# Kernel tuning notes

Measured on AMD Instinct MI355X. Metric: run time of the kernel, lower is better.

The kernel has to match this reference:

```python
import jax, jax.numpy as jnp
import numpy as np

N = 50000      # nodes
E = 800000     # edges
F_IN = 128     # n_features
H = 4          # n_heads
C1 = 64        # n_hidden (per-head out of layer 1)
C2 = 32        # n_classes (per-head out of layer 2)
NEG_SLOPE = 0.2
EPS = 1e-16


def setup_inputs() -> dict:
    key = jax.random.key(0)
    ks = jax.random.split(key, 12)
    x = jax.random.normal(ks[0], (N, F_IN), dtype=jnp.float32)
    edge_index = jax.random.randint(ks[1], (2, E), 0, N, dtype=jnp.int64)
    # layer 1 params (GATConv: shared lin for src/dst, att_src/att_dst vectors, bias)
    W1 = jax.random.normal(ks[2], (F_IN, H * C1), dtype=jnp.float32) * (1.0 / np.sqrt(F_IN))
    att_src1 = jax.random.normal(ks[3], (H, C1), dtype=jnp.float32) * 0.1
    att_dst1 = jax.random.normal(ks[4], (H, C1), dtype=jnp.float32) * 0.1
    b1 = jnp.zeros((C1,), dtype=jnp.float32)
    # layer 2 params
    W2 = jax.random.normal(ks[5], (C1, H * C2), dtype=jnp.float32) * (1.0 / np.sqrt(C1))
    att_src2 = jax.random.normal(ks[6], (H, C2), dtype=jnp.float32) * 0.1
    att_dst2 = jax.random.normal(ks[7], (H, C2), dtype=jnp.float32) * 0.1
    b2 = jnp.zeros((C2,), dtype=jnp.float32)
    return {"x": x, "edge_index": edge_index,
            "W1": W1, "att_src1": att_src1, "att_dst1": att_dst1, "b1": b1,
            "W2": W2, "att_src2": att_src2, "att_dst2": att_dst2, "b2": b2}


def gat_conv(x, src, dst, W, att_src, att_dst, b, heads, out_ch):
    """PyG GATConv with concat=False (head-averaged output)."""
    n = x.shape[0]
    h = (x @ W).reshape(n, heads, out_ch)                 # [N, H, C]
    a_s = jnp.einsum('nhc,hc->nh', h, att_src)            # [N, H]
    a_d = jnp.einsum('nhc,hc->nh', h, att_dst)            # [N, H]
    e = jax.nn.leaky_relu(a_s[src] + a_d[dst], NEG_SLOPE)  # [E, H]
    # segment softmax over edges grouped by destination node
    m = jax.ops.segment_max(e, dst, num_segments=n)        # [N, H]
    m = jnp.where(jnp.isfinite(m), m, 0.0)
    ex = jnp.exp(e - m[dst])                               # [E, H]
    denom = jax.ops.segment_sum(ex, dst, num_segments=n)   # [N, H]
    alpha = ex / (denom[dst] + EPS)                        # [E, H]
    # scatter-add aggregation of attended source features
    msg = alpha[:, :, None] * h[src]                       # [E, H, C]
    out = jax.ops.segment_sum(msg, dst, num_segments=n)    # [N, H, C]
    return out.mean(axis=1) + b                            # [N, C]


def reference(x, edge_index, W1, att_src1, att_dst1, b1, W2, att_src2, att_dst2, b2):
    src, dst = edge_index[0], edge_index[1]
    h = jax.nn.relu(gat_conv(x, src, dst, W1, att_src1, att_dst1, b1, H, C1))
    # dropout is identity in eval mode
    out = gat_conv(h, src, dst, W2, att_src2, att_dst2, b2, H, C2)
    return out
```

## Files before the change

kernel.cpp:

```cpp
#include <hip/hip_runtime.h>
#include <hip/hip_fp16.h>
#include <cstdint>
#include <cstddef>

#define N_NODES 50000
#define N_EDGES 800000
#define F_IN 128
#define H_HEADS 4
#define C1 64
#define C2 32
#define NEG_SLOPE 0.2f
#define EPS_GAT 1e-16f
#define SLOT_CAP 96
#define FILL_BPG 256
#define NODES_PER_GROUP 6250
#define CBASE ((int)0xAAAAAAAAu)

typedef _Float16 half8 __attribute__((ext_vector_type(8)));
typedef float f32x4 __attribute__((ext_vector_type(4)));

template<int K, int M>
__device__ __forceinline__ void wtrans_dev(const float* __restrict__ W,
                                           _Float16* __restrict__ Wt,
                                           _Float16* tile, int bm, int bk) {
    const int m0 = bm * 64, k0 = bk * 64;
    const int t = threadIdx.x;
    const int c = t & 63;
#pragma unroll
    for (int j = 0; j < 16; ++j) {
        int r = (t >> 6) + 4 * j;
        tile[c * 66 + r] = (_Float16)W[(size_t)(k0 + r) * M + m0 + c];
    }
    __syncthreads();
#pragma unroll
    for (int j = 0; j < 16; ++j) {
        int m_l = (t >> 6) + 4 * j;
        Wt[(size_t)(m0 + m_l) * K + k0 + c] = tile[m_l * 66 + c];
    }
}

__global__ __launch_bounds__(256) void fill_wtrans_kernel(
        const int* __restrict__ src, const int* __restrict__ dst,
        int* __restrict__ cursor, unsigned short* __restrict__ slots,
        const float* __restrict__ W1, _Float16* __restrict__ wt1,
        const float* __restrict__ W2, _Float16* __restrict__ wt2) {
    __shared__ _Float16 tile[64 * 66];
    const int b = blockIdx.x;
    if (b < 8) {
        wtrans_dev<F_IN, H_HEADS * C1>(W1, wt1, tile, b & 3, b >> 2);
    } else if (b < 10) {
        wtrans_dev<C1, H_HEADS * C2>(W2, wt2, tile, b - 8, 0);
    }
    const int g = b & 7;
    const int bg = b >> 3;
    const int dlo = g * NODES_PER_GROUP;
    const int dhi = dlo + NODES_PER_GROUP;
    const int4* dst4 = (const int4*)dst;
    const int4* src4 = (const int4*)src;
    constexpr int NV4 = N_EDGES / 4;
    for (int v = bg * 256 + (int)threadIdx.x; v < NV4; v += FILL_BPG * 256) {
        int4 d4 = dst4[v];
        int4 s4 = src4[v];
        if (d4.x >= dlo && d4.x < dhi) {
            unsigned int p = (unsigned int)(atomicAdd(&cursor[d4.x], 1) - CBASE);
            if (p < SLOT_CAP) slots[(size_t)d4.x * SLOT_CAP + p] = (unsigned short)s4.x;
        }
        if (d4.y >= dlo && d4.y < dhi) {
            unsigned int p = (unsigned int)(atomicAdd(&cursor[d4.y], 1) - CBASE);
            if (p < SLOT_CAP) slots[(size_t)d4.y * SLOT_CAP + p] = (unsigned short)s4.y;
        }
        if (d4.z >= dlo && d4.z < dhi) {
            unsigned int p = (unsigned int)(atomicAdd(&cursor[d4.z], 1) - CBASE);
            if (p < SLOT_CAP) slots[(size_t)d4.z * SLOT_CAP + p] = (unsigned short)s4.z;
        }
        if (d4.w >= dlo && d4.w < dhi) {
            unsigned int p = (unsigned int)(atomicAdd(&cursor[d4.w], 1) - CBASE);
            if (p < SLOT_CAP) slots[(size_t)d4.w * SLOT_CAP + p] = (unsigned short)s4.w;
        }
    }
}

template<int K, int M, int Hn, int C, typename InT>
__global__ __launch_bounds__(256) void gemm_att_kernel(
        const InT* __restrict__ X, const _Float16* __restrict__ Wt,
        _Float16* __restrict__ Hout,
        const float* __restrict__ atts, const float* __restrict__ attd,
        float* __restrict__ as_, float* __restrict__ ad_, int Nr) {
    constexpr int LDK = K + 8;
    constexpr int NCT = M / 64;
    constexpr int HPB = 64 / C;
    __shared__ _Float16 Ah[64 * LDK];
    __shared__ _Float16 Bt[64 * LDK];
    __shared__ _Float16 Ht[64 * 72];
    const int row0 = blockIdx.x * 64;
    const int t = threadIdx.x;
    const int wv = t >> 6;
    const int lane = t & 63;
    const int quad = lane >> 4;
    const int n16 = lane & 15;

    if constexpr (sizeof(InT) == 4) {
        constexpr int KQ = K / 4;
#pragma unroll
        for (int j = 0; j < (64 * KQ) / 256; ++j) {
            int flat = t + 256 * j;
            int r = flat / KQ, kq = flat % KQ;
            int rg = row0 + r;
            float4 v = make_float4(0.f, 0.f, 0.f, 0.f);
            if (rg < Nr) v = *(const float4*)&X[(size_t)rg * K + 4 * kq];
            _Float16 tmp[4] = {(_Float16)v.x, (_Float16)v.y, (_Float16)v.z, (_Float16)v.w};
            *(uint2*)&Ah[r * LDK + 4 * kq] = *(const uint2*)tmp;
        }
    } else {
        constexpr int KQ = K / 8;
#pragma unroll
        for (int j = 0; j < (64 * KQ) / 256; ++j) {
            int flat = t + 256 * j;
            int r = flat / KQ, kq = flat % KQ;
            int rg = row0 + r;
            uint4 v = make_uint4(0u, 0u, 0u, 0u);
            if (rg < Nr) v = *(const uint4*)&X[(size_t)rg * K + 8 * kq];
            *(uint4*)&Ah[r * LDK + 8 * kq] = v;
        }
    }
    __syncthreads();

    half8 af[K / 32];
    const _Float16* Ap = &Ah[(16 * wv + n16) * LDK + 8 * quad];
#pragma unroll
    for (int ki = 0; ki < K / 32; ++ki) af[ki] = *(const half8*)(Ap + 32 * ki);

    for (int ct = 0; ct < NCT; ++ct) {
        const int col0 = 64 * ct;
        __syncthreads();
        {
            constexpr int KQ8 = K / 8;
#pragma unroll
            for (int j = 0; j < (64 * KQ8) / 256; ++j) {
                int flat = t + 256 * j;
                int c = flat / KQ8, kq = flat % KQ8;
                uint4 v = *(const uint4*)&Wt[(size_t)(col0 + c) * K + 8 * kq];
                *(uint4*)&Bt[c * LDK + 8 * kq] = v;
            }
        }
        __syncthreads();

        f32x4 acc[4];
#pragma unroll
        for (int nf = 0; nf < 4; ++nf) acc[nf] = (f32x4){0.f, 0.f, 0.f, 0.f};
#pragma unroll
        for (int ki = 0; ki < K / 32; ++ki) {
#pragma unroll
            for (int nf = 0; nf < 4; ++nf) {
                half8 bf = *(const half8*)&Bt[(16 * nf + n16) * LDK + 32 * ki + 8 * quad];
                acc[nf] = __builtin_amdgcn_mfma_f32_16x16x32_f16(af[ki], bf, acc[nf], 0, 0, 0);
            }
        }

        float dps[HPB][4], dpd[HPB][4];
#pragma unroll
        for (int u = 0; u < HPB; ++u)
#pragma unroll
            for (int r = 0; r < 4; ++r) { dps[u][r] = 0.f; dpd[u][r] = 0.f; }
#pragma unroll
        for (int nf = 0; nf < 4; ++nf) {
            int gc = col0 + 16 * nf + n16;
            float cs = atts[gc], cd = attd[gc];
#pragma unroll
            for (int r = 0; r < 4; ++r) {
                float av = acc[nf][r];
                dps[(16 * nf) / C][r] += av * cs;
                dpd[(16 * nf) / C][r] += av * cd;
            }
        }
#pragma unroll
        for (int u = 0; u < HPB; ++u)
#pragma unroll
            for (int r = 0; r < 4; ++r) {
                float s = dps[u][r], d = dpd[u][r];
#pragma unroll
                for (int off = 1; off < 16; off <<= 1) {
                    s += __shfl_xor(s, off, 64);
                    d += __shfl_xor(d, off, 64);
                }
                dps[u][r] = s; dpd[u][r] = d;
            }
        if (n16 == 0) {
            const int h0 = col0 / C;
#pragma unroll
            for (int r = 0; r < 4; ++r) {
                int row = row0 + 16 * wv + 4 * quad + r;
                if (row < Nr) {
#pragma unroll
                    for (int u = 0; u < HPB; ++u) {
                        as_[row * Hn + h0 + u] = dps[u][r];
                        ad_[row * Hn + h0 + u] = dpd[u][r];
                    }
                }
            }
        }

#pragma unroll
        for (int nf = 0; nf < 4; ++nf)
#pragma unroll
            for (int r = 0; r < 4; ++r)
                Ht[(16 * wv + 4 * quad + r) * 72 + 16 * nf + n16] = (_Float16)acc[nf][r];
        __syncthreads();
#pragma unroll
        for (int j = 0; j < 2; ++j) {
            int chunk = t + 256 * j;
            int r = chunk >> 3, cc = chunk & 7;
            int row = row0 + r;
            if (row < Nr) {
                uint4 v = *(const uint4*)&Ht[r * 72 + 8 * cc];
                *(uint4*)&Hout[(size_t)row * M + col0 + 8 * cc] = v;
            }
        }
    }
}

template<int Hn, int C, bool RELU, bool OUT_F16>
__global__ __launch_bounds__(256) void gat_agg_kernel(
        const int* __restrict__ degp, const unsigned short* __restrict__ slots,
        const float* __restrict__ as_, const float* __restrict__ ad_,
        const _Float16* __restrict__ Hm, const float* __restrict__ bias,
        void* __restrict__ outv, int Nr) {
    constexpr int HC = Hn * C;
    constexpr int PER = HC / 16;
    constexpr int NV = PER / 8;
    int node = blockIdx.x * 4 + (threadIdx.x >> 6);
    int lane = threadIdx.x & 63;
    if (node >= Nr) return;
    const int g = lane >> 4;
    const int l = lane & 15;
    const int h = l >> 2;
    const float ad_h = ad_[node * Hn + h];

    const int dn = min(degp[node] - CBASE, SLOT_CAP);
    const int begin = node * SLOT_CAP;
    const int end = begin + dn;
    const int iters = (dn + 3) >> 2;

    float acc[PER];
#pragma unroll
    for (int t = 0; t < PER; ++t) acc[t] = 0.f;
    float wsum = 0.f;

    int idx = begin + g;
    bool okA = idx < end;
    int sA = (int)slots[okA ? idx : begin];
    float aA = as_[sA * Hn + h];
    uint4 uA[NV];
    {
        const uint4* hp = (const uint4*)(Hm + (size_t)sA * HC + l * PER);
        uA[0] = hp[0];
        if constexpr (NV == 2) uA[1] = hp[1];
    }

#pragma unroll 2
    for (int it = 0; it < iters; ++it) {
        const int j = idx + 4;
        const bool okB = j < end;
        int sB = (int)slots[okB ? j : begin];
        float aB = as_[sB * Hn + h];
        uint4 uB[NV];
        {
            const uint4* hp = (const uint4*)(Hm + (size_t)sB * HC + l * PER);
            uB[0] = hp[0];
            if constexpr (NV == 2) uB[1] = hp[1];
        }

        float logit = aA + ad_h;
        float lr = fmaxf(logit, NEG_SLOPE * logit);
        float w = okA ? __expf(lr) : 0.f;
        wsum += w;
#pragma unroll
        for (int v = 0; v < NV; ++v) {
            half8 hv = __builtin_bit_cast(half8, uA[v]);
#pragma unroll
            for (int e = 0; e < 8; ++e)
                acc[8 * v + e] = fmaf((float)hv[e], w, acc[8 * v + e]);
        }

        okA = okB; aA = aB;
        uA[0] = uB[0];
        if constexpr (NV == 2) uA[1] = uB[1];
        idx = j;
    }

#pragma unroll
    for (int t = 0; t < PER; ++t) {
        acc[t] += __shfl_xor(acc[t], 16, 64);
        acc[t] += __shfl_xor(acc[t], 32, 64);
    }
    wsum += __shfl_xor(wsum, 16, 64);
    wsum += __shfl_xor(wsum, 32, 64);
    const float inv = 1.f / (wsum + EPS_GAT);
    float val[PER];
#pragma unroll
    for (int t = 0; t < PER; ++t) {
        float v = acc[t] * inv;
        v += __shfl_xor(v, 4, 64);
        v += __shfl_xor(v, 8, 64);
        val[t] = v * (1.0f / Hn);
    }
    if (lane < 4) {
        const int c0 = lane * PER;
#pragma unroll
        for (int t = 0; t < PER; ++t) {
            float v = val[t] + bias[c0 + t];
            if (RELU) v = fmaxf(v, 0.f);
            val[t] = v;
        }
        if constexpr (OUT_F16) {
            _Float16* o = (_Float16*)outv;
            _Float16 tmp[PER];
#pragma unroll
            for (int t = 0; t < PER; ++t) tmp[t] = (_Float16)val[t];
            uint4* d4 = (uint4*)&o[(size_t)node * C + c0];
            d4[0] = *(const uint4*)&tmp[0];
            if constexpr (NV == 2) d4[1] = *(const uint4*)&tmp[8];
        } else {
            float* o = (float*)outv;
#pragma unroll
            for (int t4 = 0; t4 < PER / 4; ++t4)
                *(float4*)&o[(size_t)node * C + c0 + 4 * t4] =
                    make_float4(val[4 * t4 + 0], val[4 * t4 + 1],
                                val[4 * t4 + 2], val[4 * t4 + 3]);
        }
    }
}

extern "C" void kernel_launch(void* const* d_in, const int* in_sizes, int n_in,
                              void* d_out, int out_size, void* d_ws, size_t ws_size,
                              hipStream_t stream) {
    const float* x    = (const float*)d_in[0];
    const int*   ei   = (const int*)d_in[1];
    const float* W1   = (const float*)d_in[2];
    const float* as1w = (const float*)d_in[3];
    const float* ad1w = (const float*)d_in[4];
    const float* b1   = (const float*)d_in[5];
    const float* W2   = (const float*)d_in[6];
    const float* as2w = (const float*)d_in[7];
    const float* ad2w = (const float*)d_in[8];
    const float* b2   = (const float*)d_in[9];
    float* out = (float*)d_out;

    const int* src = ei;
    const int* dst = ei + N_EDGES;

    char* ws = (char*)d_ws;
    size_t off = 0;
    auto alloc = [&](size_t bytes) -> void* {
        void* p = ws + off;
        off = (off + bytes + 255) & ~(size_t)255;
        return p;
    };
    int*   cursor = (int*)alloc((size_t)N_NODES * 4);
    float* as1_ = (float*)alloc((size_t)N_NODES * H_HEADS * 4);
    float* ad1_ = (float*)alloc((size_t)N_NODES * H_HEADS * 4);
    float* as2_ = (float*)alloc((size_t)N_NODES * H_HEADS * 4);
    float* ad2_ = (float*)alloc((size_t)N_NODES * H_HEADS * 4);
    _Float16* h1   = (_Float16*)alloc((size_t)N_NODES * H_HEADS * C1 * 2);
    _Float16* out1 = (_Float16*)alloc((size_t)N_NODES * C1 * 2);
    _Float16* h2   = (_Float16*)alloc((size_t)N_NODES * H_HEADS * C2 * 2);
    _Float16* wt1  = (_Float16*)alloc((size_t)(H_HEADS * C1) * F_IN * 2);
    _Float16* wt2  = (_Float16*)alloc((size_t)(H_HEADS * C2) * C1 * 2);
    unsigned short* slots = (unsigned short*)alloc((size_t)N_NODES * SLOT_CAP * 2);

    fill_wtrans_kernel<<<8 * FILL_BPG, 256, 0, stream>>>(
        src, dst, cursor, slots, W1, wt1, W2, wt2);

    gemm_att_kernel<F_IN, H_HEADS * C1, H_HEADS, C1, float>
        <<<(N_NODES + 63) / 64, 256, 0, stream>>>(
            x, wt1, h1, as1w, ad1w, as1_, ad1_, N_NODES);

    gat_agg_kernel<H_HEADS, C1, true, true><<<(N_NODES + 3) / 4, 256, 0, stream>>>(
        cursor, slots, as1_, ad1_, h1, b1, (void*)out1, N_NODES);

    gemm_att_kernel<C1, H_HEADS * C2, H_HEADS, C2, _Float16>
        <<<(N_NODES + 63) / 64, 256, 0, stream>>>(
            out1, wt2, h2, as2w, ad2w, as2_, ad2_, N_NODES);

    gat_agg_kernel<H_HEADS, C2, false, false><<<(N_NODES + 3) / 4, 256, 0, stream>>>(
        cursor, slots, as2_, ad2_, h2, b2, (void*)out, N_NODES);
}
```

Measured before the change: 250.3 us.

## Fuse layer-1 GEMM with CSR slot fill into one heterogeneous launch

Splits the weight transpose into its own small kernel and merges the layer-1 GEMM+attention blocks with the edge bucket fill blocks into a single grid, where block id selects the role. The goal is to overlap the compute-bound GEMM with the atomic-heavy, memory-bound fill and save one launch boundary. In exchange, the fill blocks now carry the GEMM's shared-memory allocation, which may lower their occupancy, and a separate transpose launch is added.

```diff
diff --git a/kernel.cpp b/kernel.cpp
--- a/kernel.cpp
+++ b/kernel.cpp
@@ -14,6 +14,7 @@
 #define SLOT_CAP 96
 #define FILL_BPG 256
 #define NODES_PER_GROUP 6250
+#define GEMM1_BLOCKS 782
 #define CBASE ((int)0xAAAAAAAAu)
 
 typedef _Float16 half8 __attribute__((ext_vector_type(8)));
@@ -39,20 +40,24 @@
     }
 }
 
-__global__ __launch_bounds__(256) void fill_wtrans_kernel(
-        const int* __restrict__ src, const int* __restrict__ dst,
-        int* __restrict__ cursor, unsigned short* __restrict__ slots,
+__global__ __launch_bounds__(256) void wtrans_kernel(
         const float* __restrict__ W1, _Float16* __restrict__ wt1,
         const float* __restrict__ W2, _Float16* __restrict__ wt2) {
     __shared__ _Float16 tile[64 * 66];
     const int b = blockIdx.x;
     if (b < 8) {
         wtrans_dev<F_IN, H_HEADS * C1>(W1, wt1, tile, b & 3, b >> 2);
-    } else if (b < 10) {
+    } else {
         wtrans_dev<C1, H_HEADS * C2>(W2, wt2, tile, b - 8, 0);
     }
-    const int g = b & 7;
-    const int bg = b >> 3;
+}
+
+__device__ __forceinline__ void fill_dev(
+        const int* __restrict__ src, const int* __restrict__ dst,
+        int* __restrict__ cursor, unsigned short* __restrict__ slots,
+        int fb) {
+    const int g = (fb + (GEMM1_BLOCKS & 7)) & 7;
+    const int bg = fb >> 3;
     const int dlo = g * NODES_PER_GROUP;
     const int dhi = dlo + NODES_PER_GROUP;
     const int4* dst4 = (const int4*)dst;
@@ -81,18 +86,15 @@
 }
 
 template<int K, int M, int Hn, int C, typename InT>
-__global__ __launch_bounds__(256) void gemm_att_kernel(
+__device__ __forceinline__ void gemm_att_dev(
         const InT* __restrict__ X, const _Float16* __restrict__ Wt,
         _Float16* __restrict__ Hout,
         const float* __restrict__ atts, const float* __restrict__ attd,
-        float* __restrict__ as_, float* __restrict__ ad_, int Nr) {
+        float* __restrict__ as_, float* __restrict__ ad_, int Nr,
+        _Float16* Ah, _Float16* Bt, _Float16* Ht, int row0) {
     constexpr int LDK = K + 8;
     constexpr int NCT = M / 64;
     constexpr int HPB = 64 / C;
-    __shared__ _Float16 Ah[64 * LDK];
-    __shared__ _Float16 Bt[64 * LDK];
-    __shared__ _Float16 Ht[64 * 72];
-    const int row0 = blockIdx.x * 64;
     const int t = threadIdx.x;
     const int wv = t >> 6;
     const int lane = t & 63;
@@ -217,6 +219,40 @@
             }
         }
     }
+}
+
+__global__ __launch_bounds__(256) void gemm1_fill_kernel(
+        const float* __restrict__ x, const _Float16* __restrict__ wt1,
+        _Float16* __restrict__ h1,
+        const float* __restrict__ atts, const float* __restrict__ attd,
+        float* __restrict__ as_, float* __restrict__ ad_,
+        const int* __restrict__ src, const int* __restrict__ dst,
+        int* __restrict__ cursor, unsigned short* __restrict__ slots) {
+    constexpr int LDK = F_IN + 8;
+    __shared__ _Float16 Ah[64 * LDK];
+    __shared__ _Float16 Bt[64 * LDK];
+    __shared__ _Float16 Ht[64 * 72];
+    if (blockIdx.x < GEMM1_BLOCKS) {
+        gemm_att_dev<F_IN, H_HEADS * C1, H_HEADS, C1, float>(
+            x, wt1, h1, atts, attd, as_, ad_, N_NODES,
+            Ah, Bt, Ht, blockIdx.x * 64);
+    } else {
+        fill_dev(src, dst, cursor, slots, blockIdx.x - GEMM1_BLOCKS);
+    }
+}
+
+template<int K, int M, int Hn, int C, typename InT>
+__global__ __launch_bounds__(256) void gemm_att_kernel(
+        const InT* __restrict__ X, const _Float16* __restrict__ Wt,
+        _Float16* __restrict__ Hout,
+        const float* __restrict__ atts, const float* __restrict__ attd,
+        float* __restrict__ as_, float* __restrict__ ad_, int Nr) {
+    constexpr int LDK = K + 8;
+    __shared__ _Float16 Ah[64 * LDK];
+    __shared__ _Float16 Bt[64 * LDK];
+    __shared__ _Float16 Ht[64 * 72];
+    gemm_att_dev<K, M, Hn, C, InT>(X, Wt, Hout, atts, attd, as_, ad_, Nr,
+                                   Ah, Bt, Ht, blockIdx.x * 64);
 }
 
 template<int Hn, int C, bool RELU, bool OUT_F16>
@@ -368,18 +404,16 @@
     _Float16* wt2  = (_Float16*)alloc((size_t)(H_HEADS * C2) * C1 * 2);
     unsigned short* slots = (unsigned short*)alloc((size_t)N_NODES * SLOT_CAP * 2);
 
-    fill_wtrans_kernel<<<8 * FILL_BPG, 256, 0, stream>>>(
-        src, dst, cursor, slots, W1, wt1, W2, wt2);
-
-    gemm_att_kernel<F_IN, H_HEADS * C1, H_HEADS, C1, float>
-        <<<(N_NODES + 63) / 64, 256, 0, stream>>>(
-            x, wt1, h1, as1w, ad1w, as1_, ad1_, N_NODES);
+    wtrans_kernel<<<10, 256, 0, stream>>>(W1, wt1, W2, wt2);
+
+    gemm1_fill_kernel<<<GEMM1_BLOCKS + 8 * FILL_BPG, 256, 0, stream>>>(
+        x, wt1, h1, as1w, ad1w, as1_, ad1_, src, dst, cursor, slots);
 
     gat_agg_kernel<H_HEADS, C1, true, true><<<(N_NODES + 3) / 4, 256, 0, stream>>>(
         cursor, slots, as1_, ad1_, h1, b1, (void*)out1, N_NODES);
 
     gemm_att_kernel<C1, H_HEADS * C2, H_HEADS, C2, _Float16>
-        <<<(N_NODES + 63) / 64, 256, 0, stream>>>(
+        <<<GEMM1_BLOCKS, 256, 0, stream>>>(
             out1, wt2, h2, as2w, ad2w, as2_, ad2_, N_NODES);
 
     gat_agg_kernel<H_HEADS, C2, false, false><<<(N_NODES + 3) / 4, 256, 0, stream>>>(
```

Measured after the change: 239.3 us. 1.05x faster.
